# Performance work log

Measured on AMD Instinct MI355X. Metric: run time of the kernel, lower is better.

Reference implementation:

```python
import jax, jax.numpy as jnp
import numpy as np
import math

D_MODEL = 1024
N_HEAD = 16
D_HEAD = D_MODEL // N_HEAD
B, T = 2, 2048


def setup_inputs() -> dict:
    key = jax.random.key(0)
    k1, k2, k3, k4, k5 = jax.random.split(key, 5)
    x = jax.random.normal(k1, (B, T, D_MODEL), dtype=jnp.float32)
    # causal mask: 1 where attending allowed (lower triangular), broadcastable [1,1,T,T]
    mask = jnp.tril(jnp.ones((T, T), dtype=jnp.int32))[None, None, :, :]
    scale = 1.0 / math.sqrt(D_MODEL)
    qkv_w = jax.random.normal(k2, (D_MODEL, 3 * D_MODEL), dtype=jnp.float32) * scale
    qkv_b = jnp.zeros((3 * D_MODEL,), dtype=jnp.float32)
    proj_w = jax.random.normal(k3, (D_MODEL, D_MODEL), dtype=jnp.float32) * scale
    proj_b = jnp.zeros((D_MODEL,), dtype=jnp.float32)
    return {"x": x, "mask": mask, "qkv_w": qkv_w, "qkv_b": qkv_b,
            "proj_w": proj_w, "proj_b": proj_b}


def reference(x, mask, qkv_w, qkv_b, proj_w, proj_b):
    Bs, Ts, C = x.shape
    qkv = x @ qkv_w + qkv_b                      # [B,T,3C]
    q, k, v = jnp.split(qkv, 3, axis=-1)
    # [B,T,C] -> [B,H,T,Dh]
    def heads(t):
        return t.reshape(Bs, Ts, N_HEAD, D_HEAD).transpose(0, 2, 1, 3)
    q, k, v = heads(q), heads(k), heads(v)
    scores = jnp.einsum('bhtd,bhsd->bhts', q, k) / math.sqrt(D_HEAD)
    scores = jnp.where(mask == 0, jnp.float32(-1e9), scores)
    attn = jax.nn.softmax(scores, axis=-1)
    out = jnp.einsum('bhts,bhsd->bhtd', attn, v)  # [B,H,T,Dh]
    out = out.transpose(0, 2, 1, 3).reshape(Bs, Ts, C)
    return out @ proj_w + proj_b
```

## Files before the change

kernel.cpp:

```cpp
#include <hip/hip_runtime.h>
#include <hip/hip_bf16.h>
#include <stdint.h>

typedef float f32x4 __attribute__((ext_vector_type(4)));
typedef float f32x16 __attribute__((ext_vector_type(16)));
typedef __bf16 bf16x8 __attribute__((ext_vector_type(8)));
typedef unsigned int uint2v __attribute__((ext_vector_type(2)));

#define D_MODEL 1024
#define NHEAD 16
#define DHEAD 64
#define BATCH 2
#define SEQ 2048
#define MROWS (BATCH*SEQ)
#define N3 (3*D_MODEL)

#define SCALE_LOG2E 0.1803368801111244f

__device__ __forceinline__ unsigned short f2bf(float f) {
  unsigned int u = __float_as_uint(f);
  u += 0x7FFF + ((u >> 16) & 1);
  return (unsigned short)(u >> 16);
}

#define CVTPK(d, x, y) asm("v_cvt_pk_bf16_f32 %0, %1, %2" : "=v"(d) : "v"(x), "v"(y))
#define SWAP32(x, y) do { uint2v _r = __builtin_amdgcn_permlane32_swap((x), (y), false, false); \
                          (x) = _r[0]; (y) = _r[1]; } while (0)

__device__ __forceinline__ void gload_lds16(const void* g, void* l) {
  __builtin_amdgcn_global_load_lds(
      (const __attribute__((address_space(1))) unsigned int*)g,
      (__attribute__((address_space(3))) unsigned int*)l, 16, 0, 0);
}

__global__ __launch_bounds__(256) void prep(const float* __restrict__ x,
                                            unsigned short* __restrict__ xb,
                                            const float* __restrict__ qkvw,
                                            unsigned short* __restrict__ oq,
                                            const float* __restrict__ projw,
                                            unsigned short* __restrict__ op) {
  int bid = blockIdx.x;
  if (bid < 2048) {
    int n4 = MROWS*D_MODEL/4;
    int i = bid*256 + threadIdx.x;
    int stride = 2048*256;
    for (; i < n4; i += stride) {
      float4 f = ((const float4*)x)[i];
      ushort4 u;
      u.x = f2bf(f.x); u.y = f2bf(f.y); u.z = f2bf(f.z); u.w = f2bf(f.w);
      ((ushort4*)xb)[i] = u;
    }
    return;
  }
  __shared__ float tile[32][33];
  int id = bid - 2048;
  const float* in; unsigned short* out; int K, N, n0, k0;
  if (id < 3072) { in = qkvw;  out = oq; K = 1024; N = 3072; n0 = (id % 96)*32; k0 = (id / 96)*32; }
  else { id -= 3072; in = projw; out = op; K = 1024; N = 1024; n0 = (id % 32)*32; k0 = (id / 32)*32; }
  int tx = threadIdx.x & 31, ty = threadIdx.x >> 5;
#pragma unroll
  for (int i = 0; i < 4; ++i)
    tile[ty + 8*i][tx] = in[(size_t)(k0 + ty + 8*i)*N + n0 + tx];
  __syncthreads();
#pragma unroll
  for (int i = 0; i < 4; ++i)
    out[(size_t)(n0 + ty + 8*i)*K + k0 + tx] = f2bf(tile[tx][ty + 8*i]);
}

#define BM 128
#define BN 128
#define BK 64

__global__ __launch_bounds__(256, 3) void gemm_bt(
    const unsigned short* __restrict__ A,
    const unsigned short* __restrict__ Bt,
    const float* __restrict__ bias,
    int K, int N, int mode,
    unsigned short* __restrict__ qo,
    unsigned short* __restrict__ ko,
    unsigned short* __restrict__ vo,
    float* __restrict__ fo)
{
  __shared__ unsigned short lds_all[BM*BK + BN*BK];
  unsigned short* a_lds = lds_all;
  unsigned short* b_lds = lds_all + BM*BK;
  int tid = threadIdx.x;
  int lane = tid & 63, wid = tid >> 6;
  int wr = wid >> 1, wc = wid & 1;
  int lr = lane & 15, lh = lane >> 4;

  int bid = blockIdx.y*gridDim.x + blockIdx.x;
  int cN = gridDim.x >> 3;
  int xcd = bid & 7;
  int j = (bid >> 3) % cN;
  int m = bid / (cN << 3);
  int M0 = m*BM, N0 = (xcd*cN + j)*BN;

  int srow = tid >> 3;
  int scol = (((tid & 7) ^ ((tid >> 3) & 7)))*8;
  const unsigned short* aP = A  + (size_t)(M0 + srow)*K + scol;
  const unsigned short* bP = Bt + (size_t)(N0 + srow)*K + scol;
  char* aL = (char*)a_lds + wid*1024;
  char* bL = (char*)b_lds + wid*1024;

  int KT = K/BK;

  f32x4 acc[4][4];
#pragma unroll
  for (int i = 0; i < 4; ++i)
#pragma unroll
    for (int j2 = 0; j2 < 4; ++j2) acc[i][j2] = (f32x4){0.f, 0.f, 0.f, 0.f};

  for (int kt = 0; kt < KT; ++kt) {
    const unsigned short* ap = aP + kt*BK;
    const unsigned short* bp = bP + kt*BK;
#pragma unroll
    for (int i = 0; i < 4; ++i) {
      gload_lds16(ap + (size_t)32*i*K, aL + i*4096);
      gload_lds16(bp + (size_t)32*i*K, bL + i*4096);
    }
    __syncthreads();
#pragma unroll
    for (int ks = 0; ks < 2; ++ks) {
      bf16x8 af[4], bf[4];
#pragma unroll
      for (int mi = 0; mi < 4; ++mi)
        af[mi] = *(const bf16x8*)&a_lds[(wr*64 + mi*16 + lr)*BK + (((ks*4 + lh) ^ (lr & 7))*8)];
#pragma unroll
      for (int ni = 0; ni < 4; ++ni)
        bf[ni] = *(const bf16x8*)&b_lds[(wc*64 + ni*16 + lr)*BK + (((ks*4 + lh) ^ (lr & 7))*8)];
#pragma unroll
      for (int mi = 0; mi < 4; ++mi)
#pragma unroll
        for (int ni = 0; ni < 4; ++ni)
          acc[mi][ni] = __builtin_amdgcn_mfma_f32_16x16x32_bf16(af[mi], bf[ni], acc[mi][ni], 0, 0, 0);
    }
    __syncthreads();
  }

  if (mode == 1) {
#pragma unroll
    for (int mi = 0; mi < 4; ++mi) {
#pragma unroll
      for (int ni = 0; ni < 4; ++ni) {
        int ncol = N0 + wc*64 + ni*16 + lr;
        float bs = bias[ncol];
        int mbase = M0 + wr*64 + mi*16 + lh*4;
#pragma unroll
        for (int r = 0; r < 4; ++r)
          fo[(size_t)(mbase + r)*N + ncol] = acc[mi][ni][r] + bs;
      }
    }
    return;
  }

  int region = N0 >> 10;
  unsigned short* c = lds_all;
#pragma unroll
  for (int mi = 0; mi < 4; ++mi) {
#pragma unroll
    for (int ni = 0; ni < 4; ++ni) {
      int n = wc*64 + ni*16 + lr;
      float bs = bias[N0 + n];
#pragma unroll
      for (int r = 0; r < 4; ++r) {
        int mm = wr*64 + mi*16 + lh*4 + r;
        float v = acc[mi][ni][r] + bs;
        if (region == 0) v *= SCALE_LOG2E;
        unsigned short u = f2bf(v);
        if (region < 2)
          c[mm*128 + ((((n >> 3) ^ (mm & 7)) << 3) | (n & 7))] = u;
        else
          c[n*128 + ((((mm >> 3) ^ (n & 7)) << 3) | (mm & 7))] = u;
      }
    }
  }
  __syncthreads();

#pragma unroll
  for (int it = 0; it < 8; ++it) {
    int idx = it*256 + tid;
    int s = idx & 7;
    int chunk = idx >> 3;
    int row = chunk >> 1, half = chunk & 1;
    int4 v4 = *(const int4*)&c[row*128 + (((half*8 + s) ^ (row & 7)) << 3)];
    if (region < 2) {
      int tg = M0 + row;
      int b = tg >> 11, tt = tg & (SEQ-1);
      int h = (((N0 & 1023)) + half*64) >> 6;
      unsigned short* dst = (region == 0) ? qo : ko;
      *(int4*)(dst + (((size_t)(b*NHEAD + h))*SEQ + tt)*DHEAD + s*8) = v4;
    } else {
      int cgl = (N0 - 2*D_MODEL) + row;
      int h = cgl >> 6, d = cgl & 63;
      int tg = M0 + half*64 + s*8;
      int b = tg >> 11, tt = tg & (SEQ-1);
      *(int4*)(vo + (((size_t)(b*NHEAD + h))*DHEAD + d)*SEQ + tt) = v4;
    }
  }
}

#define NQT128 (SEQ/128)

__global__ __launch_bounds__(256, 3) void attn_fwd(
    const unsigned short* __restrict__ q,
    const unsigned short* __restrict__ kk,
    const unsigned short* __restrict__ vt,
    unsigned short* __restrict__ out)
{
  __shared__ __align__(16) char smem[2][16384];

  int tid = threadIdx.x, lane = tid & 63, wid = tid >> 6;
  int idx = blockIdx.x;
  int qt = (NQT128 - 1) - (idx >> 5);
  int bh = idx & 31;
  int b = bh >> 4, h = bh & 15;
  int q0w = qt*128 + wid*32;
  int l31 = lane & 31, hl = lane >> 5;

  const unsigned short* qb = q  + ((size_t)bh*SEQ)*DHEAD;
  const unsigned short* kb = kk + ((size_t)bh*SEQ)*DHEAD;
  const unsigned short* vb = vt + ((size_t)bh*DHEAD)*SEQ;

  int srow = lane >> 3;
  int sslot = (lane & 7) ^ srow;

  int roff[2][4];
#pragma unroll
  for (int j = 0; j < 2; ++j)
#pragma unroll
    for (int st = 0; st < 4; ++st)
      roff[j][st] = (j*32 + l31)*128 + (((2*st + hl) ^ (l31 & 7))*16);

  bf16x8 qf[4];
#pragma unroll
  for (int st = 0; st < 4; ++st)
    qf[st] = *(const bf16x8*)(qb + (size_t)(q0w + l31)*DHEAD + st*16 + hl*8);

  f32x16 o0, o1;
#pragma unroll
  for (int i = 0; i < 16; ++i) { o0[i] = 0.f; o1[i] = 0.f; }
  float l = 0.f;
  int qg = q0w + l31;

  int nkv = 2*qt + 2;

#define STAGE(bufi, kvbase) do {                                                   \
    char* kd = smem[bufi] + wid*2048;                                              \
    char* vd = smem[bufi] + 8192 + wid*2048;                                       \
    _Pragma("unroll")                                                              \
    for (int i = 0; i < 2; ++i) {                                                  \
      gload_lds16(kb + (size_t)((kvbase) + wid*16 + i*8 + srow)*DHEAD + sslot*8,   \
                  kd + i*1024);                                                    \
      gload_lds16(vb + (size_t)(wid*16 + i*8 + srow)*SEQ + (kvbase) + sslot*8,     \
                  vd + i*1024);                                                    \
    }                                                                              \
  } while (0)

  STAGE(0, 0);
  __syncthreads();

  for (int t = 0; t < nkv; ++t) {
    int cur = t & 1;
    if (t + 1 < nkv) STAGE(cur ^ 1, (t+1)*64);
    int kv0 = t*64;

    if (kv0 <= q0w + 31) {
      const char* kbase = smem[cur];
      const char* vbase = smem[cur] + 8192;

      f32x16 s0, s1;
#pragma unroll
      for (int i = 0; i < 16; ++i) { s0[i] = 0.f; s1[i] = 0.f; }

#pragma unroll
      for (int st = 0; st < 4; ++st) {
        bf16x8 k0 = *(const bf16x8*)(kbase + roff[0][st]);
        bf16x8 k1 = *(const bf16x8*)(kbase + roff[1][st]);
        s0 = __builtin_amdgcn_mfma_f32_32x32x16_bf16(k0, qf[st], s0, 0, 0, 0);
        s1 = __builtin_amdgcn_mfma_f32_32x32x16_bf16(k1, qf[st], s1, 0, 0, 0);
      }

      if (kv0 + 63 > qg - 31) {
#pragma unroll
        for (int r = 0; r < 16; ++r) {
          int kl = (r&3) + 8*(r>>2) + 4*hl;
          if (kv0 + kl      > qg) s0[r] = -1e30f;
          if (kv0 + 32 + kl > qg) s1[r] = -1e30f;
        }
      }

#pragma unroll
      for (int j = 0; j < 2; ++j) {
        const f32x16& sj = j ? s1 : s0;
        float p[16];
#pragma unroll
        for (int r = 0; r < 16; ++r) p[r] = __builtin_amdgcn_exp2f(sj[r]);
        float t0 = (p[0]+p[1]) + (p[2]+p[3]);
        float t1 = (p[4]+p[5]) + (p[6]+p[7]);
        float t2 = (p[8]+p[9]) + (p[10]+p[11]);
        float t3 = (p[12]+p[13]) + (p[14]+p[15]);
        l += (t0+t1) + (t2+t3);
        uint32_t a0,a1,a2,a3,b0,b1,b2,b3;
        CVTPK(a0, p[0],  p[1]);  CVTPK(a1, p[2],  p[3]);
        CVTPK(b0, p[4],  p[5]);  CVTPK(b1, p[6],  p[7]);
        CVTPK(a2, p[8],  p[9]);  CVTPK(a3, p[10], p[11]);
        CVTPK(b2, p[12], p[13]); CVTPK(b3, p[14], p[15]);
        SWAP32(a0, b0); SWAP32(a1, b1); SWAP32(a2, b2); SWAP32(a3, b3);
        union { uint32_t u[4]; bf16x8 v; } pf0, pf1;
        pf0.u[0]=a0; pf0.u[1]=a1; pf0.u[2]=b0; pf0.u[3]=b1;
        pf1.u[0]=a2; pf1.u[1]=a3; pf1.u[2]=b2; pf1.u[3]=b3;
        bf16x8 v00 = *(const bf16x8*)(vbase + roff[0][2*j]);
        bf16x8 v01 = *(const bf16x8*)(vbase + roff[1][2*j]);
        bf16x8 v10 = *(const bf16x8*)(vbase + roff[0][2*j + 1]);
        bf16x8 v11 = *(const bf16x8*)(vbase + roff[1][2*j + 1]);
        o0 = __builtin_amdgcn_mfma_f32_32x32x16_bf16(v00, pf0.v, o0, 0, 0, 0);
        o1 = __builtin_amdgcn_mfma_f32_32x32x16_bf16(v01, pf0.v, o1, 0, 0, 0);
        o0 = __builtin_amdgcn_mfma_f32_32x32x16_bf16(v10, pf1.v, o0, 0, 0, 0);
        o1 = __builtin_amdgcn_mfma_f32_32x32x16_bf16(v11, pf1.v, o1, 0, 0, 0);
      }
    }
    __syncthreads();
  }
#undef STAGE

  l += __shfl_xor(l, 32);
  float inv = 1.f / l;
  o0 *= inv; o1 *= inv;

  unsigned short* obuf = (unsigned short*)smem;
  int qrow = wid*32 + l31;
  int xk = (qrow & 7) << 1;
#pragma unroll
  for (int g = 0; g < 4; ++g) {
    uint32_t w0, w1;
    CVTPK(w0, o0[4*g],   o0[4*g+1]);
    CVTPK(w1, o0[4*g+2], o0[4*g+3]);
    uint2 pk0 = {w0, w1};
    *(uint2*)&obuf[qrow*64 + (((2*g + hl) ^ xk) << 2)] = pk0;
    CVTPK(w0, o1[4*g],   o1[4*g+1]);
    CVTPK(w1, o1[4*g+2], o1[4*g+3]);
    uint2 pk1 = {w0, w1};
    *(uint2*)&obuf[qrow*64 + (((8 + 2*g + hl) ^ xk) << 2)] = pk1;
  }
  __syncthreads();

#pragma unroll
  for (int it = 0; it < 4; ++it) {
    int idx2 = it*256 + tid;
    int s = idx2 & 7, row = idx2 >> 3;
    int4 v4 = *(const int4*)&obuf[row*64 + ((s ^ (row & 7)) << 3)];
    int tq = qt*128 + row;
    *(int4*)(out + ((size_t)(b*SEQ) + tq)*D_MODEL + h*DHEAD + s*8) = v4;
  }
}

extern "C" void kernel_launch(void* const* d_in, const int* in_sizes, int n_in,
                              void* d_out, int out_size, void* d_ws, size_t ws_size,
                              hipStream_t stream) {
  const float* x      = (const float*)d_in[0];
  const float* qkv_w  = (const float*)d_in[2];
  const float* qkv_b  = (const float*)d_in[3];
  const float* proj_w = (const float*)d_in[4];
  const float* proj_b = (const float*)d_in[5];

  const size_t MB = 1024*1024;
  if (ws_size < 48*MB) return;
  char* w = (char*)d_ws;
  unsigned short* xb      = (unsigned short*)(w);
  unsigned short* wqkv_t  = (unsigned short*)(w + 8*MB);
  unsigned short* wproj_t = (unsigned short*)(w + 14*MB);
  unsigned short* qbuf    = (unsigned short*)(w + 16*MB);
  unsigned short* kbuf    = (unsigned short*)(w + 24*MB);
  unsigned short* vtbuf   = (unsigned short*)(w + 32*MB);
  unsigned short* aout    = (unsigned short*)(w + 40*MB);

  prep<<<6144, 256, 0, stream>>>(x, xb, qkv_w, wqkv_t, proj_w, wproj_t);
  gemm_bt<<<dim3(N3/BN, MROWS/BM), 256, 0, stream>>>(xb, wqkv_t, qkv_b, D_MODEL, N3, 0,
                                                     qbuf, kbuf, vtbuf, nullptr);
  attn_fwd<<<dim3(32*NQT128), 256, 0, stream>>>(qbuf, kbuf, vtbuf, aout);
  gemm_bt<<<dim3(D_MODEL/BN, MROWS/BM), 256, 0, stream>>>(aout, wproj_t, proj_b, D_MODEL, D_MODEL, 1,
                                                          nullptr, nullptr, nullptr, (float*)d_out);
}
```

Measured before the change: 102.2 us.

## Split projection GEMM into smaller-tile kernel and add MFMA priority in attention

Moves the output projection into a dedicated gemm_proj kernel with 64x128 tiles, doubling the block count (512 vs 256) so more CUs are busy on the small projection GEMM. In the attention kernel, the PV accumulators are split into two independent chains to break MFMA dependency stalls, s_setprio is raised around the MFMA sections, and launch bounds drop from 3 to 2 waves per SIMD, giving more registers per thread at the cost of occupancy. The added accumulators raise register pressure, and the new projection kernel has no XCD remapping.

```diff
diff --git a/kernel.cpp b/kernel.cpp
--- a/kernel.cpp
+++ b/kernel.cpp
@@ -75,11 +75,10 @@
     const unsigned short* __restrict__ A,
     const unsigned short* __restrict__ Bt,
     const float* __restrict__ bias,
-    int K, int N, int mode,
+    int K, int N,
     unsigned short* __restrict__ qo,
     unsigned short* __restrict__ ko,
-    unsigned short* __restrict__ vo,
-    float* __restrict__ fo)
+    unsigned short* __restrict__ vo)
 {
   __shared__ unsigned short lds_all[BM*BK + BN*BK];
   unsigned short* a_lds = lds_all;
@@ -136,22 +135,6 @@
           acc[mi][ni] = __builtin_amdgcn_mfma_f32_16x16x32_bf16(af[mi], bf[ni], acc[mi][ni], 0, 0, 0);
     }
     __syncthreads();
-  }
-
-  if (mode == 1) {
-#pragma unroll
-    for (int mi = 0; mi < 4; ++mi) {
-#pragma unroll
-      for (int ni = 0; ni < 4; ++ni) {
-        int ncol = N0 + wc*64 + ni*16 + lr;
-        float bs = bias[ncol];
-        int mbase = M0 + wr*64 + mi*16 + lh*4;
-#pragma unroll
-        for (int r = 0; r < 4; ++r)
-          fo[(size_t)(mbase + r)*N + ncol] = acc[mi][ni][r] + bs;
-      }
-    }
-    return;
   }
 
   int region = N0 >> 10;
@@ -200,9 +183,83 @@
   }
 }
 
+#define PM 64
+#define PN 128
+
+__global__ __launch_bounds__(256, 2) void gemm_proj(
+    const unsigned short* __restrict__ A,
+    const unsigned short* __restrict__ Bt,
+    const float* __restrict__ bias,
+    float* __restrict__ fo)
+{
+  __shared__ unsigned short a_lds[PM*BK];
+  __shared__ unsigned short b_lds[PN*BK];
+  int tid = threadIdx.x;
+  int lane = tid & 63, wid = tid >> 6;
+  int wr = wid >> 1, wc = wid & 1;
+  int lr = lane & 15, lh = lane >> 4;
+
+  int M0 = blockIdx.y*PM, N0 = blockIdx.x*PN;
+  const int K = D_MODEL, N = D_MODEL;
+
+  int srow = tid >> 3;
+  int scol = (((tid & 7) ^ ((tid >> 3) & 7)))*8;
+  const unsigned short* aP = A  + (size_t)(M0 + srow)*K + scol;
+  const unsigned short* bP = Bt + (size_t)(N0 + srow)*K + scol;
+  char* aL = (char*)a_lds + wid*1024;
+  char* bL = (char*)b_lds + wid*1024;
+
+  f32x4 acc[2][4];
+#pragma unroll
+  for (int i = 0; i < 2; ++i)
+#pragma unroll
+    for (int j2 = 0; j2 < 4; ++j2) acc[i][j2] = (f32x4){0.f, 0.f, 0.f, 0.f};
+
+  for (int kt = 0; kt < K/BK; ++kt) {
+    const unsigned short* ap = aP + kt*BK;
+    const unsigned short* bp = bP + kt*BK;
+#pragma unroll
+    for (int i = 0; i < 2; ++i)
+      gload_lds16(ap + (size_t)32*i*K, aL + i*4096);
+#pragma unroll
+    for (int i = 0; i < 4; ++i)
+      gload_lds16(bp + (size_t)32*i*K, bL + i*4096);
+    __syncthreads();
+#pragma unroll
+    for (int ks = 0; ks < 2; ++ks) {
+      bf16x8 af[2], bf[4];
+#pragma unroll
+      for (int mi = 0; mi < 2; ++mi)
+        af[mi] = *(const bf16x8*)&a_lds[(wr*32 + mi*16 + lr)*BK + (((ks*4 + lh) ^ (lr & 7))*8)];
+#pragma unroll
+      for (int ni = 0; ni < 4; ++ni)
+        bf[ni] = *(const bf16x8*)&b_lds[(wc*64 + ni*16 + lr)*BK + (((ks*4 + lh) ^ (lr & 7))*8)];
+#pragma unroll
+      for (int mi = 0; mi < 2; ++mi)
+#pragma unroll
+        for (int ni = 0; ni < 4; ++ni)
+          acc[mi][ni] = __builtin_amdgcn_mfma_f32_16x16x32_bf16(af[mi], bf[ni], acc[mi][ni], 0, 0, 0);
+    }
+    __syncthreads();
+  }
+
+#pragma unroll
+  for (int mi = 0; mi < 2; ++mi) {
+#pragma unroll
+    for (int ni = 0; ni < 4; ++ni) {
+      int ncol = N0 + wc*64 + ni*16 + lr;
+      float bs = bias[ncol];
+      int mbase = M0 + wr*32 + mi*16 + lh*4;
+#pragma unroll
+      for (int r = 0; r < 4; ++r)
+        fo[(size_t)(mbase + r)*N + ncol] = acc[mi][ni][r] + bs;
+    }
+  }
+}
+
 #define NQT128 (SEQ/128)
 
-__global__ __launch_bounds__(256, 3) void attn_fwd(
+__global__ __launch_bounds__(256, 2) void attn_fwd(
     const unsigned short* __restrict__ q,
     const unsigned short* __restrict__ kk,
     const unsigned short* __restrict__ vt,
@@ -237,9 +294,9 @@
   for (int st = 0; st < 4; ++st)
     qf[st] = *(const bf16x8*)(qb + (size_t)(q0w + l31)*DHEAD + st*16 + hl*8);
 
-  f32x16 o0, o1;
-#pragma unroll
-  for (int i = 0; i < 16; ++i) { o0[i] = 0.f; o1[i] = 0.f; }
+  f32x16 o0a, o0b, o1a, o1b;
+#pragma unroll
+  for (int i = 0; i < 16; ++i) { o0a[i] = 0.f; o0b[i] = 0.f; o1a[i] = 0.f; o1b[i] = 0.f; }
   float l = 0.f;
   int qg = q0w + l31;
 
@@ -273,6 +330,7 @@
 #pragma unroll
       for (int i = 0; i < 16; ++i) { s0[i] = 0.f; s1[i] = 0.f; }
 
+      __builtin_amdgcn_s_setprio(1);
 #pragma unroll
       for (int st = 0; st < 4; ++st) {
         bf16x8 k0 = *(const bf16x8*)(kbase + roff[0][st]);
@@ -280,6 +338,7 @@
         s0 = __builtin_amdgcn_mfma_f32_32x32x16_bf16(k0, qf[st], s0, 0, 0, 0);
         s1 = __builtin_amdgcn_mfma_f32_32x32x16_bf16(k1, qf[st], s1, 0, 0, 0);
       }
+      __builtin_amdgcn_s_setprio(0);
 
       if (kv0 + 63 > qg - 31) {
 #pragma unroll
@@ -314,16 +373,20 @@
         bf16x8 v01 = *(const bf16x8*)(vbase + roff[1][2*j]);
         bf16x8 v10 = *(const bf16x8*)(vbase + roff[0][2*j + 1]);
         bf16x8 v11 = *(const bf16x8*)(vbase + roff[1][2*j + 1]);
-        o0 = __builtin_amdgcn_mfma_f32_32x32x16_bf16(v00, pf0.v, o0, 0, 0, 0);
-        o1 = __builtin_amdgcn_mfma_f32_32x32x16_bf16(v01, pf0.v, o1, 0, 0, 0);
-        o0 = __builtin_amdgcn_mfma_f32_32x32x16_bf16(v10, pf1.v, o0, 0, 0, 0);
-        o1 = __builtin_amdgcn_mfma_f32_32x32x16_bf16(v11, pf1.v, o1, 0, 0, 0);
+        __builtin_amdgcn_s_setprio(1);
+        o0a = __builtin_amdgcn_mfma_f32_32x32x16_bf16(v00, pf0.v, o0a, 0, 0, 0);
+        o1a = __builtin_amdgcn_mfma_f32_32x32x16_bf16(v01, pf0.v, o1a, 0, 0, 0);
+        o0b = __builtin_amdgcn_mfma_f32_32x32x16_bf16(v10, pf1.v, o0b, 0, 0, 0);
+        o1b = __builtin_amdgcn_mfma_f32_32x32x16_bf16(v11, pf1.v, o1b, 0, 0, 0);
+        __builtin_amdgcn_s_setprio(0);
       }
     }
     __syncthreads();
   }
 #undef STAGE
 
+  f32x16 o0 = o0a + o0b;
+  f32x16 o1 = o1a + o1b;
   l += __shfl_xor(l, 32);
   float inv = 1.f / l;
   o0 *= inv; o1 *= inv;
@@ -376,9 +439,8 @@
   unsigned short* aout    = (unsigned short*)(w + 40*MB);
 
   prep<<<6144, 256, 0, stream>>>(x, xb, qkv_w, wqkv_t, proj_w, wproj_t);
-  gemm_bt<<<dim3(N3/BN, MROWS/BM), 256, 0, stream>>>(xb, wqkv_t, qkv_b, D_MODEL, N3, 0,
-                                                     qbuf, kbuf, vtbuf, nullptr);
+  gemm_bt<<<dim3(N3/BN, MROWS/BM), 256, 0, stream>>>(xb, wqkv_t, qkv_b, D_MODEL, N3,
+                                                     qbuf, kbuf, vtbuf);
   attn_fwd<<<dim3(32*NQT128), 256, 0, stream>>>(qbuf, kbuf, vtbuf, aout);
-  gemm_bt<<<dim3(D_MODEL/BN, MROWS/BM), 256, 0, stream>>>(aout, wproj_t, proj_b, D_MODEL, D_MODEL, 1,
-                                                          nullptr, nullptr, nullptr, (float*)d_out);
-}
+  gemm_proj<<<dim3(D_MODEL/PN, MROWS/PM), 256, 0, stream>>>(aout, wproj_t, proj_b, (float*)d_out);
+}
```

New measurement: 100.4 us. No clear change (-1.8%).
